# Kernel tuning notes

Hardware: AMD Instinct MI355X
Metric: run time of the kernel (lower is better)

## Reference

```python
import jax, jax.numpy as jnp
import numpy as np

EPS = 1e-5  # BatchNorm eps
K_NN = 16


def _conv1d(w, b, x):
    # 1x1 Conv1d: w (O,C), x (B,C,N) -> (B,O,N)
    return jnp.einsum('oc,bcn->bon', w, x) + b[None, :, None]


def _conv2d(w, b, x):
    # 1x1 Conv2d: w (O,C), x (B,C,N,K) -> (B,O,N,K)
    return jnp.einsum('oc,bcnk->bonk', w, x) + b[None, :, None, None]


def _bn2d(x, g, bt, mu, var):
    # eval-mode BatchNorm2d over channel axis 1
    inv = g / jnp.sqrt(var + EPS)
    return x * inv[None, :, None, None] + (bt - mu * inv)[None, :, None, None]


def _group(f, idx):
    # grouping_operation: f (B,C,M), idx (B,N,K) -> (B,C,N,K)
    return jax.vmap(lambda fb, ib: fb[:, ib])(f, idx)


def _knn(query_pts, ref_pts, k):
    # query (B,N,3), ref (B,M,3) -> k nearest ref indices per query (B,N,k)
    d = (jnp.sum(query_pts ** 2, -1)[:, :, None]
         + jnp.sum(ref_pts ** 2, -1)[:, None, :]
         - 2.0 * jnp.einsum('bnc,bmc->bnm', query_pts, ref_pts))
    _, idx = jax.lax.top_k(-d, k)
    return idx


def setup_inputs() -> dict:
    key = jax.random.key(0)
    B, n, m, C, D, PH = 4, 4096, 1024, 128, 256, 64
    AH = 2 * D
    ks = iter(jax.random.split(key, 40))

    def nrm(shape, scale):
        return jax.random.normal(next(ks), shape, jnp.float32) * scale

    pos = nrm((B, 3, n), 1.0)
    return {
        'pos': pos,
        'pos_flipped': jnp.transpose(pos, (0, 2, 1)),
        'fea': nrm((B, C, n), 1.0),
        'seed': nrm((B, m, 3), 1.0),
        'seed_fea': nrm((B, C, m), 1.0),
        'w_start': nrm((D, C), C ** -0.5), 'b_start': jnp.zeros((D,), jnp.float32),
        'w_key': nrm((D, D), D ** -0.5), 'b_key': jnp.zeros((D,), jnp.float32),
        'w_value': nrm((D, D), D ** -0.5), 'b_value': jnp.zeros((D,), jnp.float32),
        'w_query': nrm((D, C), C ** -0.5), 'b_query': jnp.zeros((D,), jnp.float32),
        'pos_w1': nrm((PH, 4), 0.5), 'pos_b1': jnp.zeros((PH,), jnp.float32),
        'pos_g1': jnp.ones((PH,), jnp.float32), 'pos_beta1': jnp.zeros((PH,), jnp.float32),
        'pos_mu1': jnp.zeros((PH,), jnp.float32), 'pos_var1': jnp.ones((PH,), jnp.float32),
        'pos_w2': nrm((D, PH), PH ** -0.5), 'pos_b2': jnp.zeros((D,), jnp.float32),
        'attn_w1': nrm((AH, D), D ** -0.5), 'attn_b1': jnp.zeros((AH,), jnp.float32),
        'attn_g1': jnp.ones((AH,), jnp.float32), 'attn_beta1': jnp.zeros((AH,), jnp.float32),
        'attn_mu1': jnp.zeros((AH,), jnp.float32), 'attn_var1': jnp.ones((AH,), jnp.float32),
        'attn_w2': nrm((D, AH), AH ** -0.5), 'attn_b2': jnp.zeros((D,), jnp.float32),
        'w_end': nrm((C, D), D ** -0.5), 'b_end': jnp.zeros((C,), jnp.float32),
    }


def reference(pos, pos_flipped, fea, seed, seed_fea,
              w_start, b_start, w_key, b_key, w_value, b_value, w_query, b_query,
              pos_w1, pos_b1, pos_g1, pos_beta1, pos_mu1, pos_var1, pos_w2, pos_b2,
              attn_w1, attn_b1, attn_g1, attn_beta1, attn_mu1, attn_var1, attn_w2, attn_b2,
              w_end, b_end):
    value = _conv1d(w_start, b_start, seed_fea)                    # (B,D,m)
    idx = _knn(jax.lax.stop_gradient(pos_flipped),
               jax.lax.stop_gradient(seed), K_NN)                  # (B,n,K) no-grad topk
    key_f = _conv1d(w_key, b_key, value)
    val_f = _conv1d(w_value, b_value, value)
    query = _conv1d(w_query, b_query, fea)                         # (B,D,n)
    key_g = _group(key_f, idx)                                     # (B,D,n,K)
    qk_rel = query[:, :, :, None] - key_g
    val_g = _group(val_f, idx)                                     # (B,D,n,K)
    coord_xj = _group(jnp.transpose(seed, (0, 2, 1)), idx)         # (B,3,n,K)
    pos_rel = pos[:, :, :, None] - coord_xj                        # (B,3,n,K)
    dis = jnp.linalg.norm(pos_rel, axis=1, keepdims=True)          # (B,1,n,K)
    h = jnp.concatenate([dis, pos_rel], axis=1)                    # (B,4,n,K)
    pe = _conv2d(pos_w2, pos_b2,
                 jax.nn.relu(_bn2d(_conv2d(pos_w1, pos_b1, h),
                                   pos_g1, pos_beta1, pos_mu1, pos_var1)))  # (B,D,n,K)
    hid = jax.nn.relu(_bn2d(_conv2d(attn_w1, attn_b1, qk_rel + pe),
                            attn_g1, attn_beta1, attn_mu1, attn_var1))
    weights = jax.nn.softmax(_conv2d(attn_w2, attn_b2, hid), axis=-1)  # softmax over K
    agg = jnp.einsum('bcnk,bcnk->bcn', weights, val_g + pe)        # (B,D,n)
    return _conv1d(w_end, b_end, agg) + fea                        # (B,C,n)
```

## Files before the change

### kernel.cpp

```cpp
#include <hip/hip_runtime.h>
#include <hip/hip_bf16.h>

#define BB   4
#define NQ   4096
#define MS   1024
#define CF   128
#define DD   256
#define PHH  64
#define AHH  512
#define KNN  16
#define EPSBN 1e-5f
#define LDT  264
#define LDH  72

typedef unsigned short ushort_t;
typedef __attribute__((ext_vector_type(8))) short bf16x8;
typedef __attribute__((ext_vector_type(4))) float floatx4;

__device__ __forceinline__ float u2f(ushort_t u) {
  return __uint_as_float(((unsigned int)u) << 16);
}
__device__ __forceinline__ ushort_t f2u(float f) {
  __hip_bfloat16 h = __float2bfloat16(f);
  return *(ushort_t*)&h;
}

#define NSEG 30
struct CvtArgs {
  const void* src[NSEG];
  int cnt[NSEG];
  int off[NSEG];
};

__global__ __launch_bounds__(256) void cvt_kernel(CvtArgs a, float* __restrict__ dst,
                                                  const ushort_t* __restrict__ probe) {
  const bool f32 = (probe[0] == 0);
  const int gid = blockIdx.x * 256 + threadIdx.x;
  const int gsz = gridDim.x * 256;
  for (int s = 0; s < NSEG; ++s) {
    float* d = dst + a.off[s];
    const int n = a.cnt[s];
    if (f32) {
      const float* sp = (const float*)a.src[s];
      for (int i = gid; i < n; i += gsz) d[i] = sp[i];
    } else {
      const ushort_t* sp = (const ushort_t*)a.src[s];
      for (int i = gid; i < n; i += gsz) d[i] = u2f(sp[i]);
    }
  }
}

__global__ __launch_bounds__(256) void cvtw_kernel(
    const float* __restrict__ w1f, const float* __restrict__ w2f,
    const float* __restrict__ w2pf, const float* __restrict__ wqf,
    ushort_t* __restrict__ w1b, ushort_t* __restrict__ w2b,
    ushort_t* __restrict__ w2pb, ushort_t* __restrict__ wqb) {
  int i = blockIdx.x * 256 + threadIdx.x;
  w1b[i] = f2u(w1f[i]);
  w2b[i] = f2u(w2f[i]);
  if (i < DD * PHH) w2pb[i] = f2u(w2pf[i]);
  if (i < CF * DD) wqb[i] = f2u(wqf[i]);
}

__global__ __launch_bounds__(256) void vkv_kernel(
    const float* __restrict__ w_start, const float* __restrict__ b_start,
    const float* __restrict__ w_key, const float* __restrict__ b_key,
    const float* __restrict__ w_value, const float* __restrict__ b_value,
    const float* __restrict__ seed_fea,
    ushort_t* __restrict__ key_b, ushort_t* __restrict__ val_b) {
  __shared__ __align__(16) float s_val[4][DD];
  const int tid = threadIdx.x;
  const int b = blockIdx.x >> 8;
  const int m0 = (blockIdx.x & 255) << 2;

  float a0 = b_start[tid], a1 = a0, a2 = a0, a3 = a0;
  {
    const float* wrow = w_start + tid * CF;
    const float* colb = seed_fea + b * CF * MS + m0;
    for (int c = 0; c < CF; c += 4) {
      float4 w = *(const float4*)(wrow + c);
      float4 f0 = *(const float4*)(colb + (c + 0) * MS);
      float4 f1 = *(const float4*)(colb + (c + 1) * MS);
      float4 f2 = *(const float4*)(colb + (c + 2) * MS);
      float4 f3 = *(const float4*)(colb + (c + 3) * MS);
      a0 += w.x * f0.x + w.y * f1.x + w.z * f2.x + w.w * f3.x;
      a1 += w.x * f0.y + w.y * f1.y + w.z * f2.y + w.w * f3.y;
      a2 += w.x * f0.z + w.y * f1.z + w.z * f2.z + w.w * f3.z;
      a3 += w.x * f0.w + w.y * f1.w + w.z * f2.w + w.w * f3.w;
    }
  }
  s_val[0][tid] = a0; s_val[1][tid] = a1; s_val[2][tid] = a2; s_val[3][tid] = a3;
  __syncthreads();

  float ak[4], av[4];
#pragma unroll
  for (int i = 0; i < 4; ++i) { ak[i] = b_key[tid]; av[i] = b_value[tid]; }
  {
    const float* kr = w_key + tid * DD;
    const float* vr = w_value + tid * DD;
    for (int c = 0; c < DD; c += 4) {
      float4 ku = *(const float4*)(kr + c);
      float4 vu = *(const float4*)(vr + c);
      float4 v0 = *(const float4*)(&s_val[0][c]);
      float4 v1 = *(const float4*)(&s_val[1][c]);
      float4 v2 = *(const float4*)(&s_val[2][c]);
      float4 v3 = *(const float4*)(&s_val[3][c]);
      ak[0] += ku.x * v0.x + ku.y * v0.y + ku.z * v0.z + ku.w * v0.w;
      ak[1] += ku.x * v1.x + ku.y * v1.y + ku.z * v1.z + ku.w * v1.w;
      ak[2] += ku.x * v2.x + ku.y * v2.y + ku.z * v2.z + ku.w * v2.w;
      ak[3] += ku.x * v3.x + ku.y * v3.y + ku.z * v3.z + ku.w * v3.w;
      av[0] += vu.x * v0.x + vu.y * v0.y + vu.z * v0.z + vu.w * v0.w;
      av[1] += vu.x * v1.x + vu.y * v1.y + vu.z * v1.z + vu.w * v1.w;
      av[2] += vu.x * v2.x + vu.y * v2.y + vu.z * v2.z + vu.w * v2.w;
      av[3] += vu.x * v3.x + vu.y * v3.y + vu.z * v3.z + vu.w * v3.w;
    }
  }
#pragma unroll
  for (int i = 0; i < 4; ++i) {
    key_b[(b * MS + m0 + i) * DD + tid] = f2u(ak[i]);
    val_b[(b * MS + m0 + i) * DD + tid] = f2u(av[i]);
  }
}

__global__ __launch_bounds__(512) void knn_kernel(
    const float* __restrict__ pos_flipped, const float* __restrict__ seed,
    int* __restrict__ idx_out) {
  __shared__ float s_p[MS * 3];
  const int tid = threadIdx.x;
  const int wv = tid >> 6, ln = tid & 63;
  const int b = blockIdx.x >> 9;
  const int q = ((blockIdx.x & 511) << 3) + wv;

  for (int i = tid; i < MS * 3; i += 512) s_p[i] = seed[b * MS * 3 + i];
  __syncthreads();

  const float qx = pos_flipped[(b * NQ + q) * 3 + 0];
  const float qy = pos_flipped[(b * NQ + q) * 3 + 1];
  const float qz = pos_flipped[(b * NQ + q) * 3 + 2];
  const float q2 = qx * qx + qy * qy + qz * qz;

  unsigned long long key[16];
#pragma unroll
  for (int t = 0; t < 16; ++t) {
    int j = ln + (t << 6);
    float x = s_p[j * 3 + 0], y = s_p[j * 3 + 1], z = s_p[j * 3 + 2];
    float r2 = x * x + y * y + z * z;
    float dist = q2 + r2 - 2.0f * (qx * x + qy * y + qz * z);
    unsigned u = __float_as_uint(dist);
    u ^= (u >> 31) ? 0xFFFFFFFFu : 0x80000000u;
    key[t] = ((unsigned long long)u << 10) | (unsigned)j;
  }

#pragma unroll 1
  for (int r = 0; r < KNN; ++r) {
    unsigned long long m = key[0];
#pragma unroll
    for (int t = 1; t < 16; ++t) m = (key[t] < m) ? key[t] : m;
#pragma unroll
    for (int off = 32; off >= 1; off >>= 1) {
      unsigned lo = (unsigned)m, hi = (unsigned)(m >> 32);
      unsigned olo = __shfl_xor((int)lo, off);
      unsigned ohi = __shfl_xor((int)hi, off);
      unsigned long long o = ((unsigned long long)ohi << 32) | olo;
      m = (o < m) ? o : m;
    }
    if (ln == 0) idx_out[(b * NQ + q) * KNN + r] = (int)(m & 1023u);
#pragma unroll
    for (int t = 0; t < 16; ++t) key[t] = (key[t] == m) ? ~0ull : key[t];
  }
}

__global__ __launch_bounds__(256, 3) void fused_kernel(
    const float* __restrict__ pos, const float* __restrict__ seed,
    const void* __restrict__ fea_raw,
    const ushort_t* __restrict__ wqb, const float* __restrict__ b_query,
    const float* __restrict__ pos_w1, const float* __restrict__ pos_b1,
    const float* __restrict__ pos_g1, const float* __restrict__ pos_beta1,
    const float* __restrict__ pos_mu1, const float* __restrict__ pos_var1,
    const ushort_t* __restrict__ w2pb, const float* __restrict__ pos_b2,
    const float* __restrict__ attn_b1, const float* __restrict__ attn_g1,
    const float* __restrict__ attn_beta1, const float* __restrict__ attn_mu1,
    const float* __restrict__ attn_var1,
    const ushort_t* __restrict__ w1b, const ushort_t* __restrict__ w2b,
    const ushort_t* __restrict__ key_b, const ushort_t* __restrict__ val_b,
    const int* __restrict__ idx_in,
    const float* __restrict__ w_end, const float* __restrict__ b_end,
    void* __restrict__ out_raw, const ushort_t* __restrict__ probe) {
  __shared__ __align__(16) ushort_t s_t[64 * LDT];
  __shared__ __align__(16) ushort_t s_phb[64 * LDH];
  __shared__ __align__(16) ushort_t s_hid[64 * LDH];
  __shared__ float s_h[64 * 4];
  __shared__ int s_idx[64];

  float* s_agg = (float*)s_t;

  const int tid = threadIdx.x;
  const int wv = tid >> 6;
  const int ln = tid & 63;
  const int qu = ln >> 4, l15 = ln & 15;
  const bool f32io = (probe[0] == 0);
  const int q0 = blockIdx.x * 4;
  const int b = q0 >> 12;
  const int qn0 = q0 & (NQ - 1);

  if (tid < 64) {
    const int g = tid >> 4;
    const int qn = qn0 + g;
    const int j = idx_in[(q0 + g) * KNN + (tid & 15)];
    s_idx[tid] = j;
    float px = pos[(b * 3 + 0) * NQ + qn];
    float py = pos[(b * 3 + 1) * NQ + qn];
    float pz = pos[(b * 3 + 2) * NQ + qn];
    float rx = px - seed[(b * MS + j) * 3 + 0];
    float ry = py - seed[(b * MS + j) * 3 + 1];
    float rz = pz - seed[(b * MS + j) * 3 + 2];
    float dis = sqrtf(rx * rx + ry * ry + rz * rz);
    s_h[tid * 4 + 0] = dis;
    s_h[tid * 4 + 1] = rx;
    s_h[tid * 4 + 2] = ry;
    s_h[tid * 4 + 3] = rz;
  }
  __syncthreads();

  {
    const int vrow = tid >> 2, vc0 = (tid & 3) * 8;
    const ushort_t* src = key_b + (b * MS + s_idx[vrow]) * DD + vc0;
    ushort_t* dst = s_t + vrow * LDT + vc0;
#pragma unroll
    for (int i = 0; i < 8; ++i)
      *(bf16x8*)(dst + i * 32) = *(const bf16x8*)(src + i * 32);
  }

  {
    const int p = tid & 63, kb = tid >> 6;
    float4 w = *(const float4*)(pos_w1 + p * 4);
    float inv = pos_g1[p] * rsqrtf(pos_var1[p] + EPSBN);
    float off = pos_b1[p] * inv + pos_beta1[p] - pos_mu1[p] * inv;
#pragma unroll
    for (int i = 0; i < 16; ++i) {
      int gk = kb * 16 + i;
      float raw = w.x * s_h[gk * 4 + 0] + w.y * s_h[gk * 4 + 1] +
                  w.z * s_h[gk * 4 + 2] + w.w * s_h[gk * 4 + 3];
      s_phb[gk * LDH + p] = f2u(fmaxf(raw * inv + off, 0.0f));
    }
  }

  floatx4 accq[4];
  {
    bf16x8 afq[4];
    if (l15 < 4) {
      const int base_c = qu * 8;
      if (f32io) {
        const float* fp = (const float*)fea_raw + (size_t)b * CF * NQ + qn0 + l15;
#pragma unroll
        for (int ks = 0; ks < 4; ++ks) {
          bf16x8 v;
#pragma unroll
          for (int j = 0; j < 8; ++j)
            ((ushort_t*)&v)[j] = f2u(fp[(ks * 32 + base_c + j) * NQ]);
          afq[ks] = v;
        }
      } else {
        const ushort_t* fp = (const ushort_t*)fea_raw + (size_t)b * CF * NQ + qn0 + l15;
#pragma unroll
        for (int ks = 0; ks < 4; ++ks) {
          bf16x8 v;
#pragma unroll
          for (int j = 0; j < 8; ++j)
            ((ushort_t*)&v)[j] = fp[(ks * 32 + base_c + j) * NQ];
          afq[ks] = v;
        }
      }
    } else {
#pragma unroll
      for (int ks = 0; ks < 4; ++ks) afq[ks] = (bf16x8){0, 0, 0, 0, 0, 0, 0, 0};
    }
#pragma unroll
    for (int nt = 0; nt < 4; ++nt) accq[nt] = (floatx4){0.f, 0.f, 0.f, 0.f};
#pragma unroll
    for (int ks = 0; ks < 4; ++ks) {
#pragma unroll
      for (int nt = 0; nt < 4; ++nt) {
        const int d = wv * 64 + nt * 16 + l15;
        bf16x8 bfr = *(const bf16x8*)(wqb + d * CF + ks * 32 + qu * 8);
        accq[nt] = __builtin_amdgcn_mfma_f32_16x16x32_bf16(afq[ks], bfr, accq[nt], 0, 0, 0);
      }
    }
  }
  __syncthreads();

  {
    floatx4 accp[4][4];
#pragma unroll
    for (int mt = 0; mt < 4; ++mt)
#pragma unroll
      for (int nt = 0; nt < 4; ++nt) accp[mt][nt] = (floatx4){0.f, 0.f, 0.f, 0.f};
#pragma unroll
    for (int ks = 0; ks < 2; ++ks) {
      bf16x8 af[4];
#pragma unroll
      for (int mt = 0; mt < 4; ++mt)
        af[mt] = *(const bf16x8*)(s_phb + (mt * 16 + l15) * LDH + ks * 32 + qu * 8);
#pragma unroll
      for (int nt = 0; nt < 4; ++nt) {
        const int d = wv * 64 + nt * 16 + l15;
        bf16x8 bfr = *(const bf16x8*)(w2pb + d * PHH + ks * 32 + qu * 8);
#pragma unroll
        for (int mt = 0; mt < 4; ++mt)
          accp[mt][nt] = __builtin_amdgcn_mfma_f32_16x16x32_bf16(af[mt], bfr, accp[mt][nt], 0, 0, 0);
      }
    }
#pragma unroll
    for (int nt = 0; nt < 4; ++nt) {
      const int d = wv * 64 + nt * 16 + l15;
      const float bq = b_query[d];
      const float b2v = pos_b2[d];
#pragma unroll
      for (int mt = 0; mt < 4; ++mt) {
        const float qd = __shfl(accq[nt][mt], l15) + bq;
#pragma unroll
        for (int r = 0; r < 4; ++r) {
          const int row = mt * 16 + qu * 4 + r;
          float pe = accp[mt][nt][r] + b2v;
          float kf = u2f(s_t[row * LDT + d]);
          s_t[row * LDT + d] = f2u(qd - kf + pe);
        }
      }
    }
  }
  __syncthreads();

  floatx4 accl[4][4];
#pragma unroll
  for (int mt = 0; mt < 4; ++mt)
#pragma unroll
    for (int nt = 0; nt < 4; ++nt) accl[mt][nt] = (floatx4){0.f, 0.f, 0.f, 0.f};

  bf16x8 pw1[8];
#pragma unroll
  for (int ks = 0; ks < 8; ++ks)
    pw1[ks] = *(const bf16x8*)(w1b + (wv * 16 + l15) * DD + ks * 32 + qu * 8);

#pragma unroll 1
  for (int nc = 0; nc < 8; ++nc) {
    {
      floatx4 accb[4];
#pragma unroll
      for (int mt = 0; mt < 4; ++mt) accb[mt] = (floatx4){0.f, 0.f, 0.f, 0.f};
#pragma unroll
      for (int ks = 0; ks < 8; ++ks) {
#pragma unroll
        for (int mt = 0; mt < 4; ++mt) {
          bf16x8 af = *(const bf16x8*)(s_t + (mt * 16 + l15) * LDT + ks * 32 + qu * 8);
          accb[mt] = __builtin_amdgcn_mfma_f32_16x16x32_bf16(af, pw1[ks], accb[mt], 0, 0, 0);
        }
      }
      {
        const int ncn = (nc + 1) & 7;
#pragma unroll
        for (int ks = 0; ks < 8; ++ks)
          pw1[ks] = *(const bf16x8*)(w1b + (ncn * 64 + wv * 16 + l15) * DD + ks * 32 + qu * 8);
      }
      const int a = nc * 64 + wv * 16 + l15;
      float inv = attn_g1[a] * rsqrtf(attn_var1[a] + EPSBN);
      float off = attn_b1[a] * inv + attn_beta1[a] - attn_mu1[a] * inv;
#pragma unroll
      for (int mt = 0; mt < 4; ++mt)
#pragma unroll
        for (int r = 0; r < 4; ++r) {
          const int row = mt * 16 + qu * 4 + r;
          s_hid[row * LDH + wv * 16 + l15] = f2u(fmaxf(accb[mt][r] * inv + off, 0.0f));
        }
    }
    __syncthreads();
    {
#pragma unroll
      for (int ks = 0; ks < 2; ++ks) {
        bf16x8 af2[4];
#pragma unroll
        for (int mt = 0; mt < 4; ++mt)
          af2[mt] = *(const bf16x8*)(s_hid + (mt * 16 + l15) * LDH + ks * 32 + qu * 8);
#pragma unroll
        for (int nt = 0; nt < 4; ++nt) {
          bf16x8 bfr = *(const bf16x8*)(w2b + (wv * 64 + nt * 16 + l15) * AHH +
                                        nc * 64 + ks * 32 + qu * 8);
#pragma unroll
          for (int mt = 0; mt < 4; ++mt)
            accl[mt][nt] = __builtin_amdgcn_mfma_f32_16x16x32_bf16(af2[mt], bfr, accl[mt][nt], 0, 0, 0);
        }
      }
    }
    __syncthreads();
  }

#pragma unroll
  for (int nt = 0; nt < 4; ++nt) {
    const int c = wv * 64 + nt * 16 + l15;
    floatx4 ap[4];
#pragma unroll
    for (int mt = 0; mt < 4; ++mt) ap[mt] = (floatx4){0.f, 0.f, 0.f, 0.f};
#pragma unroll
    for (int ks = 0; ks < 2; ++ks) {
      bf16x8 bfr = *(const bf16x8*)(w2pb + c * PHH + ks * 32 + qu * 8);
#pragma unroll
      for (int mt = 0; mt < 4; ++mt) {
        bf16x8 af = *(const bf16x8*)(s_phb + (mt * 16 + l15) * LDH + ks * 32 + qu * 8);
        ap[mt] = __builtin_amdgcn_mfma_f32_16x16x32_bf16(af, bfr, ap[mt], 0, 0, 0);
      }
    }
    const float b2v = pos_b2[c];
#pragma unroll
    for (int mt = 0; mt < 4; ++mt) {
      float l0 = accl[mt][nt][0], l1 = accl[mt][nt][1];
      float l2 = accl[mt][nt][2], l3 = accl[mt][nt][3];
      float mx = fmaxf(fmaxf(l0, l1), fmaxf(l2, l3));
      mx = fmaxf(mx, __shfl_xor(mx, 16));
      mx = fmaxf(mx, __shfl_xor(mx, 32));
      float e0 = expf(l0 - mx), e1 = expf(l1 - mx);
      float e2 = expf(l2 - mx), e3 = expf(l3 - mx);
      float s = e0 + e1 + e2 + e3;
      s += __shfl_xor(s, 16);
      s += __shfl_xor(s, 32);
      const int row0 = mt * 16 + qu * 4;
      float v0 = u2f(val_b[(b * MS + s_idx[row0 + 0]) * DD + c]);
      float v1 = u2f(val_b[(b * MS + s_idx[row0 + 1]) * DD + c]);
      float v2 = u2f(val_b[(b * MS + s_idx[row0 + 2]) * DD + c]);
      float v3 = u2f(val_b[(b * MS + s_idx[row0 + 3]) * DD + c]);
      float p = e0 * (v0 + ap[mt][0] + b2v) + e1 * (v1 + ap[mt][1] + b2v) +
                e2 * (v2 + ap[mt][2] + b2v) + e3 * (v3 + ap[mt][3] + b2v);
      p += __shfl_xor(p, 16);
      p += __shfl_xor(p, 32);
      if (ln < 16) s_agg[mt * DD + c] = p / s;
    }
  }
  __syncthreads();

  {
    const int c = tid & 127;
    const int qh = tid >> 7;
    float acc0 = 0.0f, acc1 = 0.0f;
    const float* wr = w_end + c * DD;
    for (int d = 0; d < DD; d += 4) {
      float4 w4 = *(const float4*)(wr + d);
      float4 a0 = *(const float4*)(s_agg + (qh + 0) * DD + d);
      float4 a1 = *(const float4*)(s_agg + (qh + 2) * DD + d);
      acc0 += w4.x * a0.x + w4.y * a0.y + w4.z * a0.z + w4.w * a0.w;
      acc1 += w4.x * a1.x + w4.y * a1.y + w4.z * a1.z + w4.w * a1.w;
    }
    const float be = b_end[c];
#pragma unroll
    for (int t = 0; t < 2; ++t) {
      const int q = qh + t * 2;
      const float accv = (t == 0) ? acc0 : acc1;
      const int oidx = (b * CF + c) * NQ + qn0 + q;
      float fres = f32io ? ((const float*)fea_raw)[oidx]
                         : u2f(((const ushort_t*)fea_raw)[oidx]);
      float v = accv + be + fres;
      if (f32io) ((float*)out_raw)[oidx] = v;
      else ((ushort_t*)out_raw)[oidx] = f2u(v);
    }
  }
}

extern "C" void kernel_launch(void* const* d_in, const int* in_sizes, int n_in,
                              void* d_out, int out_size, void* d_ws, size_t ws_size,
                              hipStream_t stream) {
  (void)in_sizes; (void)n_in; (void)out_size; (void)ws_size;

  float* wsf = (float*)d_ws;
  ushort_t* key_b = (ushort_t*)wsf;
  ushort_t* val_b = (ushort_t*)(wsf + 524288);
  int*      idxw  = (int*)(wsf + 1048576);
  float*    nrm   = wsf + 1310720;
  ushort_t* w1b   = (ushort_t*)(wsf + 2458304);
  ushort_t* w2b   = (ushort_t*)(wsf + 2523840);
  ushort_t* w2pb  = (ushort_t*)(wsf + 2589376);
  ushort_t* wqb   = (ushort_t*)(wsf + 2597568);

  static const int seg_in[NSEG] = {0, 1, 3, 4, 5, 6, 7, 8, 9, 10, 11, 12, 13, 14,
                                   15, 16, 17, 18, 19, 20, 21, 22, 23, 24, 25, 26,
                                   27, 28, 29, 30};
  static const int seg_cnt[NSEG] = {
      49152, 49152, 12288, 524288, 32768, 256, 65536, 256, 65536, 256,
      32768, 256, 256, 64, 64, 64, 64, 64, 16384, 256,
      131072, 512, 512, 512, 512, 512, 131072, 256, 32768, 128};
  static const int seg_off[NSEG] = {
      0, 49152, 98304, 110592, 634880, 667648, 667904, 733440, 733696, 799232,
      799488, 832256, 832512, 832768, 832832, 832896, 832960, 833024, 833088, 849472,
      849728, 980800, 981312, 981824, 982336, 982848, 983360, 1114432, 1114688, 1147456};

  CvtArgs ca;
  for (int s = 0; s < NSEG; ++s) {
    ca.src[s] = d_in[seg_in[s]];
    ca.cnt[s] = seg_cnt[s];
    ca.off[s] = seg_off[s];
  }
  const ushort_t* probe = (const ushort_t*)d_in[18];

  const float* posN      = nrm + 0;
  const float* pos_flipN = nrm + 49152;
  const float* seedN     = nrm + 98304;
  const float* seed_feaN = nrm + 110592;
  const float* w_startN  = nrm + 634880;
  const float* b_startN  = nrm + 667648;
  const float* w_keyN    = nrm + 667904;
  const float* b_keyN    = nrm + 733440;
  const float* w_valueN  = nrm + 733696;
  const float* b_valueN  = nrm + 799232;
  const float* b_queryN  = nrm + 832256;
  const float* pos_w1N   = nrm + 832512;
  const float* pos_b1N   = nrm + 832768;
  const float* pos_g1N   = nrm + 832832;
  const float* pos_beta1N= nrm + 832896;
  const float* pos_mu1N  = nrm + 832960;
  const float* pos_var1N = nrm + 833024;
  const float* pos_w2N   = nrm + 833088;
  const float* pos_b2N   = nrm + 849472;
  const float* attn_w1N  = nrm + 849728;
  const float* attn_b1N  = nrm + 980800;
  const float* attn_g1N  = nrm + 981312;
  const float* attn_beta1N = nrm + 981824;
  const float* attn_mu1N = nrm + 982336;
  const float* attn_var1N= nrm + 982848;
  const float* attn_w2N  = nrm + 983360;
  const float* w_endN    = nrm + 1114688;
  const float* b_endN    = nrm + 1147456;
  const float* w_queryN  = nrm + 799488;

  cvt_kernel<<<512, 256, 0, stream>>>(ca, nrm, probe);
  cvtw_kernel<<<512, 256, 0, stream>>>(attn_w1N, attn_w2N, pos_w2N, w_queryN,
                                       w1b, w2b, w2pb, wqb);
  vkv_kernel<<<BB * MS / 4, 256, 0, stream>>>(w_startN, b_startN, w_keyN, b_keyN,
                                              w_valueN, b_valueN, seed_feaN,
                                              key_b, val_b);
  knn_kernel<<<BB * NQ / 8, 512, 0, stream>>>(pos_flipN, seedN, idxw);

  fused_kernel<<<BB * NQ / 4, 256, 0, stream>>>(
      posN, seedN, d_in[2], wqb, b_queryN,
      pos_w1N, pos_b1N, pos_g1N, pos_beta1N, pos_mu1N, pos_var1N,
      w2pb, pos_b2N,
      attn_b1N, attn_g1N, attn_beta1N, attn_mu1N, attn_var1N,
      w1b, w2b, key_b, val_b, idxw,
      w_endN, b_endN, d_out, probe);
}
```

Baseline: 781.2 us.

## Fold attention first layer into query, key, and positional weights via linearity

Uses linearity of the first attention conv: W1·(q − k + pe) is split into W1·Wq·fea, W1·key (precomputed once per seed point in a new kh_kernel), and (W1·W2p)·pos_hidden. A prep kernel builds the combined weights and bias. The per-neighbour K=256 GEMM in the fused kernel shrinks to K=64 plus gathers of precomputed 512-wide key projections. This trades per-query compute for extra gather bandwidth (512 bf16 per neighbour instead of 256) and a bf16 rounding of the combined weights. Occupancy is also raised to 4 blocks per SM now that the large shared tile is gone.

```diff
diff --git a/kernel.cpp b/kernel.cpp
--- a/kernel.cpp
+++ b/kernel.cpp
@@ -10,8 +10,8 @@
 #define AHH  512
 #define KNN  16
 #define EPSBN 1e-5f
-#define LDT  264
 #define LDH  72
+#define LKH  264
 
 typedef unsigned short ushort_t;
 typedef __attribute__((ext_vector_type(8))) short bf16x8;
@@ -52,14 +52,42 @@
 
 __global__ __launch_bounds__(256) void cvtw_kernel(
     const float* __restrict__ w1f, const float* __restrict__ w2f,
-    const float* __restrict__ w2pf, const float* __restrict__ wqf,
+    const float* __restrict__ w2pf,
     ushort_t* __restrict__ w1b, ushort_t* __restrict__ w2b,
-    ushort_t* __restrict__ w2pb, ushort_t* __restrict__ wqb) {
+    ushort_t* __restrict__ w2pb) {
   int i = blockIdx.x * 256 + threadIdx.x;
   w1b[i] = f2u(w1f[i]);
   w2b[i] = f2u(w2f[i]);
   if (i < DD * PHH) w2pb[i] = f2u(w2pf[i]);
-  if (i < CF * DD) wqb[i] = f2u(wqf[i]);
+}
+
+__global__ __launch_bounds__(128) void prep_kernel(
+    const float* __restrict__ w1f, const float* __restrict__ w2pf,
+    const float* __restrict__ wqf, const float* __restrict__ bqf,
+    const float* __restrict__ b2f, const float* __restrict__ ab1f,
+    ushort_t* __restrict__ WWb, ushort_t* __restrict__ WQHb,
+    float* __restrict__ ballf) {
+  __shared__ float s_w1[DD];
+  const int a = blockIdx.x;
+  const int t = threadIdx.x;
+  s_w1[t] = w1f[a * DD + t];
+  s_w1[t + 128] = w1f[a * DD + t + 128];
+  __syncthreads();
+  {
+    float acc = 0.f;
+    for (int d = 0; d < DD; ++d) acc += s_w1[d] * wqf[d * CF + t];
+    WQHb[a * CF + t] = f2u(acc);
+  }
+  if (t < PHH) {
+    float acc = 0.f;
+    for (int d = 0; d < DD; ++d) acc += s_w1[d] * w2pf[d * PHH + t];
+    WWb[a * PHH + t] = f2u(acc);
+  }
+  if (t == 0) {
+    float acc = ab1f[a];
+    for (int d = 0; d < DD; ++d) acc += s_w1[d] * (bqf[d] + b2f[d]);
+    ballf[a] = acc;
+  }
 }
 
 __global__ __launch_bounds__(256) void vkv_kernel(
@@ -122,6 +150,44 @@
   }
 }
 
+__global__ __launch_bounds__(256) void kh_kernel(
+    const ushort_t* __restrict__ key_b, const ushort_t* __restrict__ w1b,
+    ushort_t* __restrict__ khb) {
+  __shared__ __align__(16) ushort_t s_key[16 * LKH];
+  const int tid = threadIdx.x;
+  const int wv = tid >> 6, ln = tid & 63;
+  const int qu = ln >> 4, l15 = ln & 15;
+  const int b = blockIdx.x >> 6;
+  const int m0 = (blockIdx.x & 63) << 4;
+  {
+    const int row = tid >> 4, seg = tid & 15;
+    const ushort_t* src = key_b + (b * MS + m0 + row) * DD + seg * 16;
+    ushort_t* dst = s_key + row * LKH + seg * 16;
+    *(bf16x8*)(dst + 0) = *(const bf16x8*)(src + 0);
+    *(bf16x8*)(dst + 8) = *(const bf16x8*)(src + 8);
+  }
+  __syncthreads();
+  bf16x8 af[8];
+#pragma unroll
+  for (int ks = 0; ks < 8; ++ks)
+    af[ks] = *(const bf16x8*)(s_key + l15 * LKH + ks * 32 + qu * 8);
+  floatx4 acc[8];
+#pragma unroll
+  for (int nt = 0; nt < 8; ++nt) acc[nt] = (floatx4){0.f, 0.f, 0.f, 0.f};
+#pragma unroll
+  for (int ks = 0; ks < 8; ++ks)
+#pragma unroll
+    for (int nt = 0; nt < 8; ++nt) {
+      bf16x8 bfr = *(const bf16x8*)(w1b + (wv * 128 + nt * 16 + l15) * DD + ks * 32 + qu * 8);
+      acc[nt] = __builtin_amdgcn_mfma_f32_16x16x32_bf16(af[ks], bfr, acc[nt], 0, 0, 0);
+    }
+#pragma unroll
+  for (int nt = 0; nt < 8; ++nt)
+#pragma unroll
+    for (int r = 0; r < 4; ++r)
+      khb[(b * MS + m0 + qu * 4 + r) * AHH + wv * 128 + nt * 16 + l15] = f2u(acc[nt][r]);
+}
+
 __global__ __launch_bounds__(512) void knn_kernel(
     const float* __restrict__ pos_flipped, const float* __restrict__ seed,
     int* __restrict__ idx_out) {
@@ -170,29 +236,30 @@
   }
 }
 
-__global__ __launch_bounds__(256, 3) void fused_kernel(
+__global__ __launch_bounds__(256, 4) void fused_kernel(
     const float* __restrict__ pos, const float* __restrict__ seed,
     const void* __restrict__ fea_raw,
-    const ushort_t* __restrict__ wqb, const float* __restrict__ b_query,
     const float* __restrict__ pos_w1, const float* __restrict__ pos_b1,
     const float* __restrict__ pos_g1, const float* __restrict__ pos_beta1,
     const float* __restrict__ pos_mu1, const float* __restrict__ pos_var1,
     const ushort_t* __restrict__ w2pb, const float* __restrict__ pos_b2,
-    const float* __restrict__ attn_b1, const float* __restrict__ attn_g1,
-    const float* __restrict__ attn_beta1, const float* __restrict__ attn_mu1,
-    const float* __restrict__ attn_var1,
-    const ushort_t* __restrict__ w1b, const ushort_t* __restrict__ w2b,
-    const ushort_t* __restrict__ key_b, const ushort_t* __restrict__ val_b,
+    const float* __restrict__ attn_g1, const float* __restrict__ attn_beta1,
+    const float* __restrict__ attn_mu1, const float* __restrict__ attn_var1,
+    const float* __restrict__ ballf,
+    const ushort_t* __restrict__ WWb, const ushort_t* __restrict__ WQHb,
+    const ushort_t* __restrict__ w2b, const ushort_t* __restrict__ khb,
+    const ushort_t* __restrict__ val_b,
     const int* __restrict__ idx_in,
     const float* __restrict__ w_end, const float* __restrict__ b_end,
     void* __restrict__ out_raw, const ushort_t* __restrict__ probe) {
-  __shared__ __align__(16) ushort_t s_t[64 * LDT];
   __shared__ __align__(16) ushort_t s_phb[64 * LDH];
   __shared__ __align__(16) ushort_t s_hid[64 * LDH];
+  __shared__ __align__(16) float s_qh[4 * AHH];
+  __shared__ __align__(16) ushort_t s_feab[4 * CF];
   __shared__ float s_h[64 * 4];
   __shared__ int s_idx[64];
 
-  float* s_agg = (float*)s_t;
+  float* s_agg = s_qh;
 
   const int tid = threadIdx.x;
   const int wv = tid >> 6;
@@ -220,16 +287,25 @@
     s_h[tid * 4 + 2] = ry;
     s_h[tid * 4 + 3] = rz;
   }
-  __syncthreads();
-
-  {
-    const int vrow = tid >> 2, vc0 = (tid & 3) * 8;
-    const ushort_t* src = key_b + (b * MS + s_idx[vrow]) * DD + vc0;
-    ushort_t* dst = s_t + vrow * LDT + vc0;
-#pragma unroll
-    for (int i = 0; i < 8; ++i)
-      *(bf16x8*)(dst + i * 32) = *(const bf16x8*)(src + i * 32);
-  }
+  if (tid < 128) {
+    const int c = tid;
+    if (f32io) {
+      const float* fc = (const float*)fea_raw + (size_t)b * CF * NQ + (size_t)c * NQ + qn0;
+      float4 v = *(const float4*)fc;
+      s_feab[0 * CF + c] = f2u(v.x);
+      s_feab[1 * CF + c] = f2u(v.y);
+      s_feab[2 * CF + c] = f2u(v.z);
+      s_feab[3 * CF + c] = f2u(v.w);
+    } else {
+      const ushort_t* fc = (const ushort_t*)fea_raw + (size_t)b * CF * NQ + (size_t)c * NQ + qn0;
+      unsigned long long v = *(const unsigned long long*)fc;
+      s_feab[0 * CF + c] = (ushort_t)(v);
+      s_feab[1 * CF + c] = (ushort_t)(v >> 16);
+      s_feab[2 * CF + c] = (ushort_t)(v >> 32);
+      s_feab[3 * CF + c] = (ushort_t)(v >> 48);
+    }
+  }
+  __syncthreads();
 
   {
     const int p = tid & 63, kb = tid >> 6;
@@ -245,87 +321,29 @@
     }
   }
 
-  floatx4 accq[4];
   {
     bf16x8 afq[4];
-    if (l15 < 4) {
-      const int base_c = qu * 8;
-      if (f32io) {
-        const float* fp = (const float*)fea_raw + (size_t)b * CF * NQ + qn0 + l15;
-#pragma unroll
-        for (int ks = 0; ks < 4; ++ks) {
-          bf16x8 v;
-#pragma unroll
-          for (int j = 0; j < 8; ++j)
-            ((ushort_t*)&v)[j] = f2u(fp[(ks * 32 + base_c + j) * NQ]);
-          afq[ks] = v;
-        }
-      } else {
-        const ushort_t* fp = (const ushort_t*)fea_raw + (size_t)b * CF * NQ + qn0 + l15;
-#pragma unroll
-        for (int ks = 0; ks < 4; ++ks) {
-          bf16x8 v;
-#pragma unroll
-          for (int j = 0; j < 8; ++j)
-            ((ushort_t*)&v)[j] = fp[(ks * 32 + base_c + j) * NQ];
-          afq[ks] = v;
-        }
+#pragma unroll
+    for (int ks = 0; ks < 4; ++ks) {
+      if (l15 < 4) afq[ks] = *(const bf16x8*)(s_feab + l15 * CF + ks * 32 + qu * 8);
+      else afq[ks] = (bf16x8){0, 0, 0, 0, 0, 0, 0, 0};
+    }
+    floatx4 aq[8];
+#pragma unroll
+    for (int nt = 0; nt < 8; ++nt) aq[nt] = (floatx4){0.f, 0.f, 0.f, 0.f};
+#pragma unroll
+    for (int ks = 0; ks < 4; ++ks)
+#pragma unroll
+      for (int nt = 0; nt < 8; ++nt) {
+        bf16x8 bfr = *(const bf16x8*)(WQHb + (nt * 64 + wv * 16 + l15) * CF + ks * 32 + qu * 8);
+        aq[nt] = __builtin_amdgcn_mfma_f32_16x16x32_bf16(afq[ks], bfr, aq[nt], 0, 0, 0);
       }
-    } else {
-#pragma unroll
-      for (int ks = 0; ks < 4; ++ks) afq[ks] = (bf16x8){0, 0, 0, 0, 0, 0, 0, 0};
-    }
-#pragma unroll
-    for (int nt = 0; nt < 4; ++nt) accq[nt] = (floatx4){0.f, 0.f, 0.f, 0.f};
-#pragma unroll
-    for (int ks = 0; ks < 4; ++ks) {
-#pragma unroll
-      for (int nt = 0; nt < 4; ++nt) {
-        const int d = wv * 64 + nt * 16 + l15;
-        bf16x8 bfr = *(const bf16x8*)(wqb + d * CF + ks * 32 + qu * 8);
-        accq[nt] = __builtin_amdgcn_mfma_f32_16x16x32_bf16(afq[ks], bfr, accq[nt], 0, 0, 0);
-      }
-    }
-  }
-  __syncthreads();
-
-  {
-    floatx4 accp[4][4];
-#pragma unroll
-    for (int mt = 0; mt < 4; ++mt)
-#pragma unroll
-      for (int nt = 0; nt < 4; ++nt) accp[mt][nt] = (floatx4){0.f, 0.f, 0.f, 0.f};
-#pragma unroll
-    for (int ks = 0; ks < 2; ++ks) {
-      bf16x8 af[4];
-#pragma unroll
-      for (int mt = 0; mt < 4; ++mt)
-        af[mt] = *(const bf16x8*)(s_phb + (mt * 16 + l15) * LDH + ks * 32 + qu * 8);
-#pragma unroll
-      for (int nt = 0; nt < 4; ++nt) {
-        const int d = wv * 64 + nt * 16 + l15;
-        bf16x8 bfr = *(const bf16x8*)(w2pb + d * PHH + ks * 32 + qu * 8);
-#pragma unroll
-        for (int mt = 0; mt < 4; ++mt)
-          accp[mt][nt] = __builtin_amdgcn_mfma_f32_16x16x32_bf16(af[mt], bfr, accp[mt][nt], 0, 0, 0);
-      }
-    }
-#pragma unroll
-    for (int nt = 0; nt < 4; ++nt) {
-      const int d = wv * 64 + nt * 16 + l15;
-      const float bq = b_query[d];
-      const float b2v = pos_b2[d];
-#pragma unroll
-      for (int mt = 0; mt < 4; ++mt) {
-        const float qd = __shfl(accq[nt][mt], l15) + bq;
-#pragma unroll
-        for (int r = 0; r < 4; ++r) {
-          const int row = mt * 16 + qu * 4 + r;
-          float pe = accp[mt][nt][r] + b2v;
-          float kf = u2f(s_t[row * LDT + d]);
-          s_t[row * LDT + d] = f2u(qd - kf + pe);
-        }
-      }
+    if (qu == 0) {
+#pragma unroll
+      for (int nt = 0; nt < 8; ++nt)
+#pragma unroll
+        for (int r = 0; r < 4; ++r)
+          s_qh[r * AHH + nt * 64 + wv * 16 + l15] = aq[nt][r];
     }
   }
   __syncthreads();
@@ -335,11 +353,6 @@
   for (int mt = 0; mt < 4; ++mt)
 #pragma unroll
     for (int nt = 0; nt < 4; ++nt) accl[mt][nt] = (floatx4){0.f, 0.f, 0.f, 0.f};
-
-  bf16x8 pw1[8];
-#pragma unroll
-  for (int ks = 0; ks < 8; ++ks)
-    pw1[ks] = *(const bf16x8*)(w1b + (wv * 16 + l15) * DD + ks * 32 + qu * 8);
 
 #pragma unroll 1
   for (int nc = 0; nc < 8; ++nc) {
@@ -348,29 +361,28 @@
 #pragma unroll
       for (int mt = 0; mt < 4; ++mt) accb[mt] = (floatx4){0.f, 0.f, 0.f, 0.f};
 #pragma unroll
-      for (int ks = 0; ks < 8; ++ks) {
+      for (int ks = 0; ks < 2; ++ks) {
+        bf16x8 bw = *(const bf16x8*)(WWb + (nc * 64 + wv * 16 + l15) * PHH + ks * 32 + qu * 8);
 #pragma unroll
         for (int mt = 0; mt < 4; ++mt) {
-          bf16x8 af = *(const bf16x8*)(s_t + (mt * 16 + l15) * LDT + ks * 32 + qu * 8);
-          accb[mt] = __builtin_amdgcn_mfma_f32_16x16x32_bf16(af, pw1[ks], accb[mt], 0, 0, 0);
+          bf16x8 af = *(const bf16x8*)(s_phb + (mt * 16 + l15) * LDH + ks * 32 + qu * 8);
+          accb[mt] = __builtin_amdgcn_mfma_f32_16x16x32_bf16(af, bw, accb[mt], 0, 0, 0);
         }
-      }
-      {
-        const int ncn = (nc + 1) & 7;
-#pragma unroll
-        for (int ks = 0; ks < 8; ++ks)
-          pw1[ks] = *(const bf16x8*)(w1b + (ncn * 64 + wv * 16 + l15) * DD + ks * 32 + qu * 8);
       }
       const int a = nc * 64 + wv * 16 + l15;
       float inv = attn_g1[a] * rsqrtf(attn_var1[a] + EPSBN);
-      float off = attn_b1[a] * inv + attn_beta1[a] - attn_mu1[a] * inv;
-#pragma unroll
-      for (int mt = 0; mt < 4; ++mt)
+      float offc = ballf[a] * inv + attn_beta1[a] - attn_mu1[a] * inv;
+#pragma unroll
+      for (int mt = 0; mt < 4; ++mt) {
+        const float qhv = s_qh[mt * AHH + a];
 #pragma unroll
         for (int r = 0; r < 4; ++r) {
           const int row = mt * 16 + qu * 4 + r;
-          s_hid[row * LDH + wv * 16 + l15] = f2u(fmaxf(accb[mt][r] * inv + off, 0.0f));
+          float khv = u2f(khb[(b * MS + s_idx[row]) * AHH + a]);
+          float raw = accb[mt][r] + qhv - khv;
+          s_hid[row * LDH + wv * 16 + l15] = f2u(fmaxf(raw * inv + offc, 0.0f));
         }
+      }
     }
     __syncthreads();
     {
@@ -475,7 +487,10 @@
   ushort_t* w1b   = (ushort_t*)(wsf + 2458304);
   ushort_t* w2b   = (ushort_t*)(wsf + 2523840);
   ushort_t* w2pb  = (ushort_t*)(wsf + 2589376);
-  ushort_t* wqb   = (ushort_t*)(wsf + 2597568);
+  ushort_t* khb   = (ushort_t*)(wsf + 2613952);
+  ushort_t* WWb   = (ushort_t*)(wsf + 3662528);
+  ushort_t* WQHb  = (ushort_t*)(wsf + 3678912);
+  float*    ballf = wsf + 3711680;
 
   static const int seg_in[NSEG] = {0, 1, 3, 4, 5, 6, 7, 8, 9, 10, 11, 12, 13, 14,
                                    15, 16, 17, 18, 19, 20, 21, 22, 23, 24, 25, 26,
@@ -507,6 +522,7 @@
   const float* b_keyN    = nrm + 733440;
   const float* w_valueN  = nrm + 733696;
   const float* b_valueN  = nrm + 799232;
+  const float* w_queryN  = nrm + 799488;
   const float* b_queryN  = nrm + 832256;
   const float* pos_w1N   = nrm + 832512;
   const float* pos_b1N   = nrm + 832768;
@@ -525,21 +541,24 @@
   const float* attn_w2N  = nrm + 983360;
   const float* w_endN    = nrm + 1114688;
   const float* b_endN    = nrm + 1147456;
-  const float* w_queryN  = nrm + 799488;
 
   cvt_kernel<<<512, 256, 0, stream>>>(ca, nrm, probe);
-  cvtw_kernel<<<512, 256, 0, stream>>>(attn_w1N, attn_w2N, pos_w2N, w_queryN,
-                                       w1b, w2b, w2pb, wqb);
+  cvtw_kernel<<<512, 256, 0, stream>>>(attn_w1N, attn_w2N, pos_w2N,
+                                       w1b, w2b, w2pb);
+  prep_kernel<<<512, 128, 0, stream>>>(attn_w1N, pos_w2N, w_queryN,
+                                       b_queryN, pos_b2N, attn_b1N,
+                                       WWb, WQHb, ballf);
   vkv_kernel<<<BB * MS / 4, 256, 0, stream>>>(w_startN, b_startN, w_keyN, b_keyN,
                                               w_valueN, b_valueN, seed_feaN,
                                               key_b, val_b);
+  kh_kernel<<<BB * MS / 16, 256, 0, stream>>>(key_b, w1b, khb);
   knn_kernel<<<BB * NQ / 8, 512, 0, stream>>>(pos_flipN, seedN, idxw);
 
   fused_kernel<<<BB * NQ / 4, 256, 0, stream>>>(
-      posN, seedN, d_in[2], wqb, b_queryN,
+      posN, seedN, d_in[2],
       pos_w1N, pos_b1N, pos_g1N, pos_beta1N, pos_mu1N, pos_var1N,
       w2pb, pos_b2N,
-      attn_b1N, attn_g1N, attn_beta1N, attn_mu1N, attn_var1N,
-      w1b, w2b, key_b, val_b, idxw,
+      attn_g1N, attn_beta1N, attn_mu1N, attn_var1N,
+      ballf, WWb, WQHb, w2b, khb, val_b, idxw,
       w_endN, b_endN, d_out, probe);
 }
```

New measurement: 747.6 us, median of 2. -4.3%, faster.
